# Kernel optimization log

Measured on AMD Instinct MI355X. Metric: run time of the kernel, lower is better.

The kernel has to match this reference:

```python
import jax, jax.numpy as jnp
import numpy as np

N = 128            # particles
NR = N * (N - 1)   # fully-connected directed edges = 16256
FPRIME = 32        # attention projection dim
F = 16             # input features per particle
B = 64             # batch


def _edge_indices(n):
    # Reproduce assign_matrices: itertools.product order, skip self-loops.
    r, s = np.meshgrid(np.arange(n), np.arange(n), indexing='ij')
    r, s = r.ravel(), s.ravel()
    keep = r != s
    return r[keep].astype(np.int32), s[keep].astype(np.int32)


def setup_inputs() -> dict:
    key = jax.random.key(0)
    k1, k2, k3 = jax.random.split(key, 3)
    x = jax.random.normal(k1, (B, F, N), dtype=jnp.float32)
    w = jax.random.normal(k2, (FPRIME, F), dtype=jnp.float32) * 0.05  # 'random_normal' init
    a = jax.random.normal(k3, (1, 2 * FPRIME), dtype=jnp.float32) * 0.05
    recv, send = _edge_indices(N)
    return {"x": x, "w": w, "a": a,
            "recv": jnp.asarray(recv), "send": jnp.asarray(send)}


def reference(x, w, a, recv, send):
    # wh[b,n,g] = sum_f x[b,f,n] * w[g,f]   (tf.tensordot(inputs, w, [1,1]))
    wh = jnp.einsum('bfn,gf->bng', x, w)            # (B, N, Fprime)
    # tensordot(wh, Rr/Rs) with one-hot Rr/Rs == gather by receiver/sender index
    whi = wh[:, recv, :]                            # (B, Nr, Fprime)
    whj = wh[:, send, :]                            # (B, Nr, Fprime)
    # a @ concat([whi, whj], feat axis) == a1 @ whi + a2 @ whj
    a1, a2 = a[0, :FPRIME], a[0, FPRIME:]
    out = whi @ a1 + whj @ a2                        # (B, Nr)
    return out[:, :, None]                           # (B, Nr, 1)
```

## Files before the change

### kernel.cpp

```cpp
#include <hip/hip_runtime.h>

#define BATCH 64
#define FDIM  16
#define NDIM  128
#define FP    32
#define NEDGE (NDIM * (NDIM - 1))
#define NEDGE4 (NEDGE / 4)

__global__ __launch_bounds__(256) void gat_edge_fused(
    const float* __restrict__ x,
    const float* __restrict__ w,
    const float* __restrict__ a,
    const int*   __restrict__ recv,
    const int*   __restrict__ send,
    float*       __restrict__ out)
{
    __shared__ float v1s[FDIM];
    __shared__ float v2s[FDIM];
    __shared__ float s1s[NDIM];
    __shared__ float s2s[NDIM];

    const int b = blockIdx.y;
    const int t = threadIdx.x;

    if (t < 2 * FDIM) {
        const int f = t & (FDIM - 1);
        const float* av = a + ((t < FDIM) ? 0 : FP);
        float acc = 0.f;
#pragma unroll
        for (int g = 0; g < FP; ++g)
            acc += av[g] * w[g * FDIM + f];
        if (t < FDIM) v1s[f] = acc;
        else          v2s[f] = acc;
    }
    __syncthreads();

    if (t < NDIM) {
        const float* xb = x + (size_t)b * FDIM * NDIM + t;
        float acc1 = 0.f, acc2 = 0.f;
#pragma unroll
        for (int f = 0; f < FDIM; ++f) {
            const float xv = xb[f * NDIM];
            acc1 += xv * v1s[f];
            acc2 += xv * v2s[f];
        }
        s1s[t] = acc1;
        s2s[t] = acc2;
    }
    __syncthreads();

    const int e4 = blockIdx.x * blockDim.x + t;
    if (e4 < NEDGE4) {
        const int4 r = ((const int4*)recv)[e4];
        const int4 s = ((const int4*)send)[e4];
        float4 o;
        o.x = s1s[r.x] + s2s[s.x];
        o.y = s1s[r.y] + s2s[s.y];
        o.z = s1s[r.z] + s2s[s.z];
        o.w = s1s[r.w] + s2s[s.w];
        ((float4*)(out + (size_t)b * NEDGE))[e4] = o;
    }
}

extern "C" void kernel_launch(void* const* d_in, const int* in_sizes, int n_in,
                              void* d_out, int out_size, void* d_ws, size_t ws_size,
                              hipStream_t stream) {
    const float* x    = (const float*)d_in[0];
    const float* w    = (const float*)d_in[1];
    const float* a    = (const float*)d_in[2];
    const int*   recv = (const int*)d_in[3];
    const int*   send = (const int*)d_in[4];
    float*       out  = (float*)d_out;

    dim3 grid((NEDGE4 + 255) / 256, BATCH);
    gat_edge_fused<<<grid, 256, 0, stream>>>(x, w, a, recv, send, out);
}
```

Baseline: 63.70 us.

## Compute edge indices arithmetically and fold projection vector into shuffles

```diff
diff --git a/kernel.cpp b/kernel.cpp
--- a/kernel.cpp
+++ b/kernel.cpp
@@ -11,53 +11,49 @@
     const float* __restrict__ x,
     const float* __restrict__ w,
     const float* __restrict__ a,
-    const int*   __restrict__ recv,
-    const int*   __restrict__ send,
     float*       __restrict__ out)
 {
-    __shared__ float v1s[FDIM];
-    __shared__ float v2s[FDIM];
     __shared__ float s1s[NDIM];
     __shared__ float s2s[NDIM];
 
     const int b = blockIdx.y;
     const int t = threadIdx.x;
+    const int lane = t & 63;
 
-    if (t < 2 * FDIM) {
-        const int f = t & (FDIM - 1);
-        const float* av = a + ((t < FDIM) ? 0 : FP);
-        float acc = 0.f;
+    const int f0 = lane & 15;
+    const float* av = a + ((lane & 16) ? FP : 0);
+    float vv = 0.f;
 #pragma unroll
-        for (int g = 0; g < FP; ++g)
-            acc += av[g] * w[g * FDIM + f];
-        if (t < FDIM) v1s[f] = acc;
-        else          v2s[f] = acc;
+    for (int g = 0; g < FP; ++g)
+        vv += av[g] * w[g * FDIM + f0];
+
+    const int node = t & 127;
+    const int base = (t >> 7) << 4;
+    const float* xb = x + (size_t)b * (FDIM * NDIM) + node;
+    float acc = 0.f;
+#pragma unroll
+    for (int f = 0; f < FDIM; ++f) {
+        const float vf = __shfl(vv, base + f);
+        acc += xb[f * NDIM] * vf;
     }
+    if (t < 128) s1s[node] = acc;
+    else         s2s[node] = acc;
     __syncthreads();
 
-    if (t < NDIM) {
-        const float* xb = x + (size_t)b * FDIM * NDIM + t;
-        float acc1 = 0.f, acc2 = 0.f;
-#pragma unroll
-        for (int f = 0; f < FDIM; ++f) {
-            const float xv = xb[f * NDIM];
-            acc1 += xv * v1s[f];
-            acc2 += xv * v2s[f];
-        }
-        s1s[t] = acc1;
-        s2s[t] = acc2;
-    }
-    __syncthreads();
-
-    const int e4 = blockIdx.x * blockDim.x + t;
+    const int e4 = blockIdx.x * 256 + t;
     if (e4 < NEDGE4) {
-        const int4 r = ((const int4*)recv)[e4];
-        const int4 s = ((const int4*)send)[e4];
+        int e = e4 * 4;
+        int r = e / 127;
+        int k = e - r * 127;
+        float s1v = s1s[r];
         float4 o;
-        o.x = s1s[r.x] + s2s[s.x];
-        o.y = s1s[r.y] + s2s[s.y];
-        o.z = s1s[r.z] + s2s[s.z];
-        o.w = s1s[r.w] + s2s[s.w];
+        o.x = s1v + s2s[k + (k >= r)];
+        if (++k == 127) { k = 0; s1v = s1s[++r]; }
+        o.y = s1v + s2s[k + (k >= r)];
+        if (++k == 127) { k = 0; s1v = s1s[++r]; }
+        o.z = s1v + s2s[k + (k >= r)];
+        if (++k == 127) { k = 0; s1v = s1s[++r]; }
+        o.w = s1v + s2s[k + (k >= r)];
         ((float4*)(out + (size_t)b * NEDGE))[e4] = o;
     }
 }
@@ -65,13 +61,11 @@
 extern "C" void kernel_launch(void* const* d_in, const int* in_sizes, int n_in,
                               void* d_out, int out_size, void* d_ws, size_t ws_size,
                               hipStream_t stream) {
-    const float* x    = (const float*)d_in[0];
-    const float* w    = (const float*)d_in[1];
-    const float* a    = (const float*)d_in[2];
-    const int*   recv = (const int*)d_in[3];
-    const int*   send = (const int*)d_in[4];
-    float*       out  = (float*)d_out;
+    const float* x = (const float*)d_in[0];
+    const float* w = (const float*)d_in[1];
+    const float* a = (const float*)d_in[2];
+    float*     out = (float*)d_out;
 
     dim3 grid((NEDGE4 + 255) / 256, BATCH);
-    gat_edge_fused<<<grid, 256, 0, stream>>>(x, w, a, recv, send, out);
+    gat_edge_fused<<<grid, 256, 0, stream>>>(x, w, a, out);
 }
```

Result: no change. 64.95 us (+2.0%).
